# Optimization experiments

Measured on AMD Instinct MI355X. Metric: run time of the kernel, lower is better.

Reference implementation:

```python
import jax, jax.numpy as jnp
import numpy as np

N_NODES = 25000
N_EDGES = 400000
HIDDEN = 256
NUM_FILTERS = 256
NUM_GAUSSIANS = 50
CUTOFF = 10.0


def ssp(x):
    # ShiftedSoftplus: softplus(x) - log(2)
    return jax.nn.softplus(x) - jnp.log(2.0).astype(x.dtype)


def setup_inputs() -> dict:
    key = jax.random.key(0)
    ks = jax.random.split(key, 12)
    s = 0.05
    return {
        "h": jax.random.normal(ks[0], (N_NODES, HIDDEN), dtype=jnp.float32),
        "pos": jax.random.uniform(ks[1], (N_NODES, 3), dtype=jnp.float32) * CUTOFF,
        "lin1_w": jax.random.normal(ks[2], (HIDDEN, NUM_FILTERS), dtype=jnp.float32) * s,
        "lin2_w": jax.random.normal(ks[3], (NUM_FILTERS, HIDDEN), dtype=jnp.float32) * s,
        "lin2_b": jnp.zeros((HIDDEN,), dtype=jnp.float32),
        "mlp_w1": jax.random.normal(ks[4], (NUM_GAUSSIANS, NUM_FILTERS), dtype=jnp.float32) * s,
        "mlp_b1": jnp.zeros((NUM_FILTERS,), dtype=jnp.float32),
        "mlp_w2": jax.random.normal(ks[5], (NUM_FILTERS, NUM_FILTERS), dtype=jnp.float32) * s,
        "mlp_b2": jnp.zeros((NUM_FILTERS,), dtype=jnp.float32),
        "lin_w": jax.random.normal(ks[6], (HIDDEN, HIDDEN), dtype=jnp.float32) * s,
        "lin_b": jnp.zeros((HIDDEN,), dtype=jnp.float32),
        "edge_index": jax.random.randint(ks[7], (2, N_EDGES), 0, N_NODES, dtype=jnp.int32),
    }


def reference(h, pos, lin1_w, lin2_w, lin2_b, mlp_w1, mlp_b1, mlp_w2, mlp_b2,
              lin_w, lin_b, edge_index):
    row, col = edge_index[0], edge_index[1]  # source, target (PyG convention)

    # edge distances
    diff = pos[row] - pos[col]                       # [E, 3]
    edge_weight = jnp.linalg.norm(diff, axis=-1)     # [E]

    # GaussianSmearing(0, cutoff, num_gaussians)
    offset = jnp.linspace(0.0, CUTOFF, NUM_GAUSSIANS, dtype=h.dtype)
    coeff = -0.5 / (offset[1] - offset[0]) ** 2
    edge_attr = jnp.exp(coeff * (edge_weight[:, None] - offset) ** 2)  # [E, G]

    # CFConv filter network * cosine cutoff
    W = ssp(edge_attr @ mlp_w1 + mlp_b1) @ mlp_w2 + mlp_b2             # [E, F]
    C = 0.5 * (jnp.cos(edge_weight * (jnp.pi / CUTOFF)) + 1.0)         # [E]
    W = W * C[:, None]

    # gather - multiply - scatter-add
    x = h @ lin1_w                                                     # [N, F] (no bias)
    msg = x[row] * W                                                   # [E, F]
    agg = jax.ops.segment_sum(msg, col, num_segments=N_NODES)          # [N, F]

    x = agg @ lin2_w + lin2_b
    x = ssp(x)
    h_update = x @ lin_w + lin_b                                       # [N, H]
    return (h_update, pos)
```

## Files before the change

### kernel.cpp

```cpp
#include <hip/hip_runtime.h>
#include <hip/hip_bf16.h>

#define N_NODES 25000
#define N_EDGES 400000
#define NTILES (N_EDGES / 32)

typedef __attribute__((ext_vector_type(8))) __bf16 bf16x8;
typedef __attribute__((ext_vector_type(4))) float f32x4;
typedef __attribute__((ext_vector_type(2))) unsigned uint32x2;

#define BAR() do {                                          \
    asm volatile("s_waitcnt lgkmcnt(0)" ::: "memory");      \
    __builtin_amdgcn_s_barrier();                           \
    asm volatile("" ::: "memory");                          \
} while (0)

static __device__ __forceinline__ unsigned short bfbits(float f) {
    __bf16 h = (__bf16)f;
    return __builtin_bit_cast(unsigned short, h);
}
static __device__ __forceinline__ float bf2f(unsigned short u) {
    return __builtin_bit_cast(float, ((unsigned)u) << 16);
}
static __device__ __forceinline__ float ssp_f(float x) {
    const float t = __builtin_amdgcn_exp2f(x * 1.44269504f);
    return 0.69314718f * (__builtin_amdgcn_logf(1.f + t) - 1.f);
}

template<int EPI, int OBF, int ABF>
__global__ __launch_bounds__(256, 2)
void node_gemm(const void* __restrict__ Av, const float* __restrict__ B,
               const float* __restrict__ bias, void* __restrict__ outv, int M)
{
    extern __shared__ char lds[];
    const int tid  = threadIdx.x;
    const int half = blockIdx.x & 1;
    const int jblk = half << 7;
    const int row0 = (blockIdx.x >> 1) << 7;

    {
        const int j   = tid & 127;
        const int k2b = (tid >> 7) << 6;
        for (int i = 0; i < 64; ++i) {
            const int k = (k2b + i) * 2;
            const float b0 = B[k * 256 + jblk + j];
            const float b1 = B[(k + 1) * 256 + jblk + j];
            const unsigned pack = (unsigned)bfbits(b0) | ((unsigned)bfbits(b1) << 16);
            *(unsigned*)(lds + ((j * 512 + k * 2) ^ ((j & 7) << 4))) = pack;
        }
    }
    __syncthreads();

    const int wave = tid >> 6;
    const int l    = tid & 63;
    const int lrow = l & 15;
    const int kg   = (l >> 4) << 3;

    f32x4 acc[8][2];
    const f32x4 z4 = {0.f, 0.f, 0.f, 0.f};
    #pragma unroll
    for (int m = 0; m < 8; ++m) { acc[m][0] = z4; acc[m][1] = z4; }

    #pragma unroll
    for (int ks = 0; ks < 8; ++ks) {
        const int k0 = (ks << 5) + kg;
        bf16x8 bfr[2];
        #pragma unroll
        for (int n = 0; n < 2; ++n) {
            const int jl = (wave << 5) + (n << 4) + lrow;
            bfr[n] = *(const bf16x8*)(lds + ((jl * 512 + k0 * 2) ^ ((jl & 7) << 4)));
        }
        #pragma unroll
        for (int m = 0; m < 8; ++m) {
            const int row = row0 + (m << 4) + lrow;
            bf16x8 af;
            if (row < M) {
                if (ABF) {
                    af = *(const bf16x8*)((const __bf16*)Av + row * 256 + k0);
                } else {
                    const float* ap = (const float*)Av + row * 256 + k0;
                    const f32x4 a0 = *(const f32x4*)(ap);
                    const f32x4 a1 = *(const f32x4*)(ap + 4);
                    #pragma unroll
                    for (int b = 0; b < 4; ++b) { af[b] = (__bf16)a0[b]; af[b + 4] = (__bf16)a1[b]; }
                }
            } else {
                #pragma unroll
                for (int b = 0; b < 8; ++b) af[b] = (__bf16)0.f;
            }
            acc[m][0] = __builtin_amdgcn_mfma_f32_16x16x32_bf16(af, bfr[0], acc[m][0], 0, 0, 0);
            acc[m][1] = __builtin_amdgcn_mfma_f32_16x16x32_bf16(af, bfr[1], acc[m][1], 0, 0, 0);
        }
    }

    #pragma unroll
    for (int m = 0; m < 8; ++m) {
        #pragma unroll
        for (int n = 0; n < 2; ++n) {
            const int j = jblk + (wave << 5) + (n << 4) + lrow;
            float bv = 0.f;
            if (EPI) bv = bias[j];
            #pragma unroll
            for (int r = 0; r < 4; ++r) {
                const int row = row0 + (m << 4) + ((l >> 4) << 2) + r;
                if (row < M) {
                    float v = acc[m][n][r] + bv;
                    if (EPI == 1) v = ssp_f(v);
                    if (OBF) ((unsigned short*)outv)[row * 256 + j] = bfbits(v);
                    else     ((float*)outv)[row * 256 + j] = v;
                }
            }
        }
    }
}

__global__ void hist_kernel(const int* __restrict__ ei, int* __restrict__ hist)
{
    const int i = blockIdx.x * 256 + threadIdx.x;
    if (i < N_EDGES) atomicAdd(&hist[ei[N_EDGES + i]], 1);
}

__global__ void scan_kernel(int* __restrict__ hist)
{
    __shared__ int part[1024];
    const int t  = threadIdx.x;
    const int CH = (N_NODES + 1023) / 1024;
    const int lo = t * CH;
    const int hi = (lo + CH < N_NODES) ? lo + CH : N_NODES;
    int s = 0;
    for (int i = lo; i < hi; ++i) s += hist[i];
    part[t] = s;
    __syncthreads();
    for (int off = 1; off < 1024; off <<= 1) {
        const int v = part[t];
        const int u = (t >= off) ? part[t - off] : 0;
        __syncthreads();
        part[t] = v + u;
        __syncthreads();
    }
    int base = (t == 0) ? 0 : part[t - 1];
    for (int i = lo; i < hi; ++i) { const int v = hist[i]; hist[i] = base; base += v; }
}

__global__ void scatter_meta(const int* __restrict__ ei, const float* __restrict__ pos,
                             int* __restrict__ hist, float4* __restrict__ meta,
                             float* __restrict__ out_pos)
{
    const int i = blockIdx.x * 256 + threadIdx.x;
    if (i >= N_EDGES) return;
    if (i < N_NODES * 3) out_pos[i] = pos[i];
    const int r = ei[i];
    const int c = ei[N_EDGES + i];
    const float dx = pos[r * 3 + 0] - pos[c * 3 + 0];
    const float dy = pos[r * 3 + 1] - pos[c * 3 + 1];
    const float dz = pos[r * 3 + 2] - pos[c * 3 + 2];
    const float d  = __fsqrt_rn(dx * dx + dy * dy + dz * dz);
    const float C  = 0.5f * (__cosf(d * 0.31415926535f) + 1.f);
    const int p = atomicAdd(&hist[c], 1);
    float4 m;
    m.x = d; m.y = C;
    m.z = __int_as_float(r); m.w = __int_as_float(c);
    meta[p] = m;
}

__global__ __launch_bounds__(256, 2)
void edge_kernel(const float4* __restrict__ meta,
                 const float* __restrict__ w1, const float* __restrict__ b1,
                 const float* __restrict__ w2, const float* __restrict__ b2,
                 const unsigned short* __restrict__ xb, float* __restrict__ agg)
{
    extern __shared__ char lds[];
    char* w2t = lds;
    char* rb  = lds + 65536;
    char* gsp = rb + 12288;
    int* colsm = (int*)(rb + 8192);

    const int tid   = threadIdx.x;
    const int wave  = tid >> 6;
    const int l     = tid & 63;
    const int lrow  = l & 15;
    const int g     = l >> 4;
    const int kg    = g << 3;
    const int half  = blockIdx.x & 1;
    const int jblk  = half << 7;
    const int group = blockIdx.x >> 1;

    {
        const int j   = tid & 127;
        const int k2b = (tid >> 7) << 6;
        for (int i = 0; i < 64; ++i) {
            const int k = (k2b + i) * 2;
            const float v0 = w2[k * 256 + jblk + j];
            const float v1 = w2[(k + 1) * 256 + jblk + j];
            const unsigned pack = (unsigned)bfbits(v0) | ((unsigned)bfbits(v1) << 16);
            *(unsigned*)(w2t + ((j * 512 + k * 2) ^ ((j & 7) << 4))) = pack;
        }
    }

    const float dlt    = 10.f / 49.f;
    const float coeff2 = (-0.5f / (dlt * dlt)) * 1.44269504f;
    bf16x8 w1f[4][2];
    #pragma unroll
    for (int n = 0; n < 4; ++n)
        #pragma unroll
        for (int ks = 0; ks < 2; ++ks) {
            bf16x8 v;
            #pragma unroll
            for (int b = 0; b < 8; ++b) {
                const int k = (ks << 5) + kg + b;
                const int j = (wave << 6) + (n << 4) + lrow;
                v[b] = (k < 50) ? (__bf16)w1[k * 256 + j] : (__bf16)0.f;
            }
            w1f[n][ks] = v;
        }
    float b1v[4], b2v[2];
    #pragma unroll
    for (int n = 0; n < 4; ++n) b1v[n] = b1[(wave << 6) + (n << 4) + lrow];
    #pragma unroll
    for (int n = 0; n < 2; ++n) b2v[n] = b2[jblk + (wave << 5) + (n << 4) + lrow];

    BAR();

    const f32x4 z4 = {0.f, 0.f, 0.f, 0.f};
    const int CH = (NTILES + 255) / 256;
    const int t0 = group * CH;
    int t1 = t0 + CH; if (t1 > NTILES) t1 = NTILES;

    const int ge  = tid >> 3;
    const int gkb = (tid & 7) << 3;

    int   rprev  = -1;
    float rs     = 0.f;
    int   rfirst = 1;
    float* aj    = agg + jblk + (tid & 127);

    float4 mv = meta[(t0 << 5) + (l & 31)];

    for (int t = t0; t < t1; ++t) {
        const float d  = mv.x;
        const float Cc = mv.y;
        const int   r  = __float_as_int(mv.z);
        const int   c  = __float_as_int(mv.w);
        if (t + 1 < t1) mv = meta[((t + 1) << 5) + (l & 31)];

        float xv[2][2][4];
        #pragma unroll
        for (int m = 0; m < 2; ++m)
            #pragma unroll
            for (int r4 = 0; r4 < 4; ++r4) {
                const int e  = (m << 4) + (g << 2) + r4;
                const int re = __shfl(r, e, 64);
                #pragma unroll
                for (int n = 0; n < 2; ++n) {
                    const int jloc = (wave << 5) + (n << 4) + lrow;
                    xv[m][n][r4] = bf2f(xb[re * 256 + jblk + jloc]);
                }
            }

        const float gd = __shfl(d, ge, 64);
        bf16x8 gv;
        #pragma unroll
        for (int b = 0; b < 8; ++b) {
            const int k = gkb + b;
            float gval = 0.f;
            if (k < 50) {
                const float u = gd - (float)k * dlt;
                gval = __builtin_amdgcn_exp2f(coeff2 * u * u);
            }
            gv[b] = (__bf16)gval;
        }
        *(bf16x8*)(gsp + ((ge * 128 + (gkb << 1)) ^ ((ge & 7) << 4))) = gv;
        BAR();

        bf16x8 af[2][2];
        #pragma unroll
        for (int m = 0; m < 2; ++m) {
            const int e = (m << 4) + lrow;
            #pragma unroll
            for (int ks = 0; ks < 2; ++ks)
                af[m][ks] = *(const bf16x8*)(gsp + ((e * 128 + ((ks << 5) + kg) * 2) ^ ((e & 7) << 4)));
        }
        f32x4 acc1[2][4];
        #pragma unroll
        for (int m = 0; m < 2; ++m)
            #pragma unroll
            for (int n = 0; n < 4; ++n) acc1[m][n] = z4;
        #pragma unroll
        for (int ks = 0; ks < 2; ++ks)
            #pragma unroll
            for (int m = 0; m < 2; ++m)
                #pragma unroll
                for (int n = 0; n < 4; ++n)
                    acc1[m][n] = __builtin_amdgcn_mfma_f32_16x16x32_bf16(af[m][ks], w1f[n][ks], acc1[m][n], 0, 0, 0);
        BAR();

        #pragma unroll
        for (int m = 0; m < 2; ++m)
            #pragma unroll
            for (int n = 0; n < 4; ++n)
                #pragma unroll
                for (int r4 = 0; r4 < 4; ++r4) {
                    const int e = (m << 4) + (g << 2) + r4;
                    const int k = (wave << 6) + (n << 4) + lrow;
                    const float v = ssp_f(acc1[m][n][r4] + b1v[n]);
                    *(__bf16*)(rb + ((e * 512 + k * 2) ^ ((e & 7) << 4))) = (__bf16)v;
                }
        BAR();

        f32x4 acc2[2][2];
        #pragma unroll
        for (int m = 0; m < 2; ++m) { acc2[m][0] = z4; acc2[m][1] = z4; }
        #pragma unroll
        for (int ks = 0; ks < 8; ++ks) {
            const int k0 = (ks << 5) + kg;
            bf16x8 bfr[2];
            #pragma unroll
            for (int n = 0; n < 2; ++n) {
                const int jl = (wave << 5) + (n << 4) + lrow;
                bfr[n] = *(const bf16x8*)(w2t + ((jl * 512 + k0 * 2) ^ ((jl & 7) << 4)));
            }
            #pragma unroll
            for (int m = 0; m < 2; ++m) {
                const int e = (m << 4) + lrow;
                const bf16x8 a = *(const bf16x8*)(rb + ((e * 512 + k0 * 2) ^ ((e & 7) << 4)));
                #pragma unroll
                for (int n = 0; n < 2; ++n)
                    acc2[m][n] = __builtin_amdgcn_mfma_f32_16x16x32_bf16(a, bfr[n], acc2[m][n], 0, 0, 0);
            }
        }
        BAR();

        #pragma unroll
        for (int m = 0; m < 2; ++m) {
            const int base_e = (m << 4) + (g << 2);
            #pragma unroll
            for (int n = 0; n < 2; ++n) {
                const int jloc = (wave << 5) + (n << 4) + lrow;
                float vv[4];
                #pragma unroll
                for (int r4 = 0; r4 < 4; ++r4) {
                    const int e  = base_e + r4;
                    const float Ce = __shfl(Cc, e, 64);
                    vv[r4] = (acc2[m][n][r4] + b2v[n]) * Ce * xv[m][n][r4];
                }
                uint32x2 pk;
                pk[0] = (unsigned)bfbits(vv[0]) | ((unsigned)bfbits(vv[1]) << 16);
                pk[1] = (unsigned)bfbits(vv[2]) | ((unsigned)bfbits(vv[3]) << 16);
                *(uint32x2*)(rb + ((jloc * 64 + (base_e << 1)) ^ ((jloc & 7) << 4))) = pk;
            }
        }
        if (tid < 32) colsm[tid] = c;
        BAR();

        if (tid < 128) {
            const int j = tid;
            const bf16x8 q0 = *(const bf16x8*)(rb + ((j * 64 +  0) ^ ((j & 7) << 4)));
            const bf16x8 q1 = *(const bf16x8*)(rb + ((j * 64 + 16) ^ ((j & 7) << 4)));
            const bf16x8 q2 = *(const bf16x8*)(rb + ((j * 64 + 32) ^ ((j & 7) << 4)));
            const bf16x8 q3 = *(const bf16x8*)(rb + ((j * 64 + 48) ^ ((j & 7) << 4)));
            #pragma unroll
            for (int e = 0; e < 32; ++e) {
                const float v = (float)(e < 8 ? q0[e] : e < 16 ? q1[e - 8] :
                                        e < 24 ? q2[e - 16] : q3[e - 24]);
                const int ce = colsm[e];
                if (ce != rprev) {
                    if (rprev >= 0) {
                        if (rfirst) { atomicAdd(aj + rprev * 256, rs); rfirst = 0; }
                        else        { aj[rprev * 256] = rs; }
                    }
                    rs = 0.f; rprev = ce;
                }
                rs += v;
            }
        }
    }
    if (tid < 128 && rprev >= 0) atomicAdd(aj + rprev * 256, rs);
}

extern "C" void kernel_launch(void* const* d_in, const int* in_sizes, int n_in,
                              void* d_out, int out_size, void* d_ws, size_t ws_size,
                              hipStream_t stream)
{
    const float* h      = (const float*)d_in[0];
    const float* pos    = (const float*)d_in[1];
    const float* lin1_w = (const float*)d_in[2];
    const float* lin2_w = (const float*)d_in[3];
    const float* lin2_b = (const float*)d_in[4];
    const float* mlp_w1 = (const float*)d_in[5];
    const float* mlp_b1 = (const float*)d_in[6];
    const float* mlp_w2 = (const float*)d_in[7];
    const float* mlp_b2 = (const float*)d_in[8];
    const float* lin_w  = (const float*)d_in[9];
    const float* lin_b  = (const float*)d_in[10];
    const int*   ei     = (const int*)d_in[11];
    float* out = (float*)d_out;

    unsigned short* xb  = (unsigned short*)d_ws;
    float*  agg  = (float*)((char*)d_ws + 12800000);
    float4* meta = (float4*)((char*)d_ws + 38400000);
    int*    hist = (int*)((char*)d_ws + 44800000);

    (void)hipFuncSetAttribute((const void*)edge_kernel,
                              hipFuncAttributeMaxDynamicSharedMemorySize, 81920);
    (void)hipFuncSetAttribute((const void*)node_gemm<0, 1, 0>,
                              hipFuncAttributeMaxDynamicSharedMemorySize, 65536);
    (void)hipFuncSetAttribute((const void*)node_gemm<1, 1, 0>,
                              hipFuncAttributeMaxDynamicSharedMemorySize, 65536);
    (void)hipFuncSetAttribute((const void*)node_gemm<2, 0, 1>,
                              hipFuncAttributeMaxDynamicSharedMemorySize, 65536);

    (void)hipMemsetAsync(agg, 0, (size_t)N_NODES * 256 * sizeof(float), stream);
    (void)hipMemsetAsync(hist, 0, (size_t)N_NODES * sizeof(int), stream);

    const dim3 blk(256);
    const int mt = (N_NODES + 127) / 128;
    const int eb = (N_EDGES + 255) / 256;

    node_gemm<0, 1, 0><<<dim3(mt * 2), blk, 65536, stream>>>(h, lin1_w, nullptr, xb, N_NODES);

    hist_kernel<<<dim3(eb), blk, 0, stream>>>(ei, hist);
    scan_kernel<<<dim3(1), dim3(1024), 0, stream>>>(hist);
    scatter_meta<<<dim3(eb), blk, 0, stream>>>(ei, pos, hist, meta, out + N_NODES * 256);

    edge_kernel<<<dim3(512), blk, 81920, stream>>>(meta, mlp_w1, mlp_b1,
                                                   mlp_w2, mlp_b2, xb, agg);

    node_gemm<1, 1, 0><<<dim3(mt * 2), blk, 65536, stream>>>(agg, lin2_w, lin2_b, xb, N_NODES);
    node_gemm<2, 0, 1><<<dim3(mt * 2), blk, 65536, stream>>>(xb, lin_w, lin_b, out, N_NODES);
}
```

Baseline: 447.2 us.

## Pre-transpose node GEMM weights to bf16 and read B fragments from global

Adds a small kernel that converts and transposes the three node-GEMM weight matrices to bf16 once per call. The node GEMMs no longer stage the full B half into 64KB of LDS in every block. Each block now covers 64 rows by all 256 columns, with each wave owning 64 columns, and reads B fragments straight from global memory, relying on L2 hits. This drops the per-block LDS fill, its barrier and the LDS occupancy limit, and halves redundant reads of A across column halves. The cost is one extra launch and more global or L2 traffic for B.

```diff
diff --git a/kernel.cpp b/kernel.cpp
--- a/kernel.cpp
+++ b/kernel.cpp
@@ -27,51 +27,51 @@
     return 0.69314718f * (__builtin_amdgcn_logf(1.f + t) - 1.f);
 }
 
+__global__ void convt_kernel(const float* __restrict__ b0, const float* __restrict__ b1,
+                             const float* __restrict__ b2, __bf16* __restrict__ t0,
+                             __bf16* __restrict__ t1, __bf16* __restrict__ t2)
+{
+    const int i   = blockIdx.x * 256 + threadIdx.x;
+    const int mat = i >> 16;
+    const int e   = i & 65535;
+    const int k   = e >> 8;
+    const int j   = e & 255;
+    const float* src = (mat == 0) ? b0 : (mat == 1) ? b1 : b2;
+    __bf16*      dst = (mat == 0) ? t0 : (mat == 1) ? t1 : t2;
+    dst[j * 256 + k] = (__bf16)src[k * 256 + j];
+}
+
 template<int EPI, int OBF, int ABF>
 __global__ __launch_bounds__(256, 2)
-void node_gemm(const void* __restrict__ Av, const float* __restrict__ B,
+void node_gemm(const void* __restrict__ Av, const __bf16* __restrict__ Bt,
                const float* __restrict__ bias, void* __restrict__ outv, int M)
 {
-    extern __shared__ char lds[];
     const int tid  = threadIdx.x;
-    const int half = blockIdx.x & 1;
-    const int jblk = half << 7;
-    const int row0 = (blockIdx.x >> 1) << 7;
-
-    {
-        const int j   = tid & 127;
-        const int k2b = (tid >> 7) << 6;
-        for (int i = 0; i < 64; ++i) {
-            const int k = (k2b + i) * 2;
-            const float b0 = B[k * 256 + jblk + j];
-            const float b1 = B[(k + 1) * 256 + jblk + j];
-            const unsigned pack = (unsigned)bfbits(b0) | ((unsigned)bfbits(b1) << 16);
-            *(unsigned*)(lds + ((j * 512 + k * 2) ^ ((j & 7) << 4))) = pack;
-        }
-    }
-    __syncthreads();
-
     const int wave = tid >> 6;
     const int l    = tid & 63;
     const int lrow = l & 15;
     const int kg   = (l >> 4) << 3;
-
-    f32x4 acc[8][2];
+    const int row0 = blockIdx.x << 6;
+    const int jw   = wave << 6;
+
+    f32x4 acc[4][4];
     const f32x4 z4 = {0.f, 0.f, 0.f, 0.f};
     #pragma unroll
-    for (int m = 0; m < 8; ++m) { acc[m][0] = z4; acc[m][1] = z4; }
+    for (int m = 0; m < 4; ++m)
+        #pragma unroll
+        for (int n = 0; n < 4; ++n) acc[m][n] = z4;
 
     #pragma unroll
     for (int ks = 0; ks < 8; ++ks) {
         const int k0 = (ks << 5) + kg;
-        bf16x8 bfr[2];
-        #pragma unroll
-        for (int n = 0; n < 2; ++n) {
-            const int jl = (wave << 5) + (n << 4) + lrow;
-            bfr[n] = *(const bf16x8*)(lds + ((jl * 512 + k0 * 2) ^ ((jl & 7) << 4)));
-        }
-        #pragma unroll
-        for (int m = 0; m < 8; ++m) {
+        bf16x8 bfr[4];
+        #pragma unroll
+        for (int n = 0; n < 4; ++n) {
+            const int jl = jw + (n << 4) + lrow;
+            bfr[n] = *(const bf16x8*)(Bt + jl * 256 + k0);
+        }
+        #pragma unroll
+        for (int m = 0; m < 4; ++m) {
             const int row = row0 + (m << 4) + lrow;
             bf16x8 af;
             if (row < M) {
@@ -88,16 +88,17 @@
                 #pragma unroll
                 for (int b = 0; b < 8; ++b) af[b] = (__bf16)0.f;
             }
-            acc[m][0] = __builtin_amdgcn_mfma_f32_16x16x32_bf16(af, bfr[0], acc[m][0], 0, 0, 0);
-            acc[m][1] = __builtin_amdgcn_mfma_f32_16x16x32_bf16(af, bfr[1], acc[m][1], 0, 0, 0);
+            #pragma unroll
+            for (int n = 0; n < 4; ++n)
+                acc[m][n] = __builtin_amdgcn_mfma_f32_16x16x32_bf16(af, bfr[n], acc[m][n], 0, 0, 0);
         }
     }
 
     #pragma unroll
-    for (int m = 0; m < 8; ++m) {
-        #pragma unroll
-        for (int n = 0; n < 2; ++n) {
-            const int j = jblk + (wave << 5) + (n << 4) + lrow;
+    for (int m = 0; m < 4; ++m) {
+        #pragma unroll
+        for (int n = 0; n < 4; ++n) {
+            const int j = jw + (n << 4) + lrow;
             float bv = 0.f;
             if (EPI) bv = bias[j];
             #pragma unroll
@@ -399,24 +400,23 @@
     float*  agg  = (float*)((char*)d_ws + 12800000);
     float4* meta = (float4*)((char*)d_ws + 38400000);
     int*    hist = (int*)((char*)d_ws + 44800000);
+    __bf16* bt0  = (__bf16*)((char*)d_ws + 44900000);
+    __bf16* bt1  = bt0 + 65536;
+    __bf16* bt2  = bt1 + 65536;
 
     (void)hipFuncSetAttribute((const void*)edge_kernel,
                               hipFuncAttributeMaxDynamicSharedMemorySize, 81920);
-    (void)hipFuncSetAttribute((const void*)node_gemm<0, 1, 0>,
-                              hipFuncAttributeMaxDynamicSharedMemorySize, 65536);
-    (void)hipFuncSetAttribute((const void*)node_gemm<1, 1, 0>,
-                              hipFuncAttributeMaxDynamicSharedMemorySize, 65536);
-    (void)hipFuncSetAttribute((const void*)node_gemm<2, 0, 1>,
-                              hipFuncAttributeMaxDynamicSharedMemorySize, 65536);
 
     (void)hipMemsetAsync(agg, 0, (size_t)N_NODES * 256 * sizeof(float), stream);
     (void)hipMemsetAsync(hist, 0, (size_t)N_NODES * sizeof(int), stream);
 
     const dim3 blk(256);
-    const int mt = (N_NODES + 127) / 128;
+    const int mt = (N_NODES + 63) / 64;
     const int eb = (N_EDGES + 255) / 256;
 
-    node_gemm<0, 1, 0><<<dim3(mt * 2), blk, 65536, stream>>>(h, lin1_w, nullptr, xb, N_NODES);
+    convt_kernel<<<dim3(768), blk, 0, stream>>>(lin1_w, lin2_w, lin_w, bt0, bt1, bt2);
+
+    node_gemm<0, 1, 0><<<dim3(mt), blk, 0, stream>>>(h, bt0, nullptr, xb, N_NODES);
 
     hist_kernel<<<dim3(eb), blk, 0, stream>>>(ei, hist);
     scan_kernel<<<dim3(1), dim3(1024), 0, stream>>>(hist);
@@ -425,6 +425,6 @@
     edge_kernel<<<dim3(512), blk, 81920, stream>>>(meta, mlp_w1, mlp_b1,
                                                    mlp_w2, mlp_b2, xb, agg);
 
-    node_gemm<1, 1, 0><<<dim3(mt * 2), blk, 65536, stream>>>(agg, lin2_w, lin2_b, xb, N_NODES);
-    node_gemm<2, 0, 1><<<dim3(mt * 2), blk, 65536, stream>>>(xb, lin_w, lin_b, out, N_NODES);
-}
+    node_gemm<1, 1, 0><<<dim3(mt), blk, 0, stream>>>(agg, bt1, lin2_b, xb, N_NODES);
+    node_gemm<2, 0, 1><<<dim3(mt), blk, 0, stream>>>(xb, bt2, lin_b, out, N_NODES);
+}
```

Measured after the change: 420.4 us. 1.06x faster.
